# Kernel tuning notes

Hardware: AMD Instinct MI355X
Metric: run time of the kernel (lower is better)

Reference implementation:

```python
import jax, jax.numpy as jnp
import numpy as np

D_MODEL = 2048
N_HEADS = 16
HEAD_DIM = D_MODEL // N_HEADS
B, L = 2, 2048
ROPE_BASE = 10000.0
NEG_INF = -1e30


def _rope_cache(seq_len, head_dim):
    inv_freq = 1.0 / (ROPE_BASE ** (np.arange(0, head_dim, 2, dtype=np.float32) / head_dim))
    t = np.arange(seq_len, dtype=np.float32)
    freqs = np.outer(t, inv_freq)                      # (L, hd/2)
    emb = np.concatenate([freqs, freqs], axis=-1)      # (L, hd)
    return jnp.asarray(np.cos(emb)), jnp.asarray(np.sin(emb))


def setup_inputs() -> dict:
    key = jax.random.key(0)
    kx, kq, ko, kl = jax.random.split(key, 4)
    x = jax.random.normal(kx, (B, L, D_MODEL), dtype=jnp.float32)
    w_qkv = jax.random.normal(kq, (3 * D_MODEL, D_MODEL), dtype=jnp.float32) / np.sqrt(D_MODEL)
    w_out = jax.random.normal(ko, (D_MODEL, D_MODEL), dtype=jnp.float32) / np.sqrt(D_MODEL)
    # key-padding style keep-mask: keep first `lengths[b]` tokens (pos 0 always kept)
    lengths = jax.random.randint(kl, (B,), L // 2, L + 1)
    attn_keep_mask = jnp.arange(L)[None, :] < lengths[:, None]
    cos, sin = _rope_cache(L, HEAD_DIM)
    return {"x": x, "attn_keep_mask": attn_keep_mask, "cos": cos, "sin": sin,
            "w_qkv": w_qkv, "w_out": w_out}


def _rotate_half(t):
    h = t.shape[-1] // 2
    return jnp.concatenate([-t[..., h:], t[..., :h]], axis=-1)


def _apply_rope(t, cos, sin):
    # t: (B, H, L, hd); cos/sin: (L, hd)
    return t * cos[None, None] + _rotate_half(t) * sin[None, None]


def reference(x, attn_keep_mask, cos, sin, w_qkv, w_out):
    Bv, Lv, Dv = x.shape
    qkv = jnp.einsum('bld,ed->ble', x, w_qkv)                      # (B, L, 3D)
    q, k, v = jnp.split(qkv, 3, axis=-1)
    def heads(t):
        return t.reshape(Bv, Lv, N_HEADS, HEAD_DIM).transpose(0, 2, 1, 3)  # (B,H,L,hd)
    q, k, v = heads(q), heads(k), heads(v)
    q = _apply_rope(q, cos, sin)
    k = _apply_rope(k, cos, sin)
    scale = 1.0 / np.sqrt(HEAD_DIM)
    scores = jnp.einsum('bhqd,bhkd->bhqk', q, k) * scale            # (B,H,L,L)
    causal = jnp.tril(jnp.ones((Lv, Lv), dtype=bool))               # (L,L)
    allowed = causal[None, None] & attn_keep_mask[:, None, None, :]  # keep keys
    scores = jnp.where(allowed, scores, NEG_INF)
    probs = jax.nn.softmax(scores, axis=-1)
    attn = jnp.einsum('bhqk,bhkd->bhqd', probs, v)                  # (B,H,L,hd)
    out = attn.transpose(0, 2, 1, 3).reshape(Bv, Lv, Dv)
    out = jnp.where(attn_keep_mask[:, :, None], out, 0.0)
    return jnp.einsum('bld,ed->ble', out, w_out)
```

## Files before the change

kernel.cpp:

```cpp
#include <hip/hip_runtime.h>

typedef unsigned short u16;
typedef u16 u16x8 __attribute__((ext_vector_type(8)));
typedef u16 u16x4 __attribute__((ext_vector_type(4)));
typedef __bf16 bf16x8_t __attribute__((ext_vector_type(8)));
typedef float f32x4 __attribute__((ext_vector_type(4)));

#define GLOBAL_AS __attribute__((address_space(1)))
#define LDS_AS __attribute__((address_space(3)))

__device__ __forceinline__ float bf2f(u16 v) {
    return __uint_as_float(((unsigned int)v) << 16);
}
__device__ __forceinline__ u16 f2bf(float f) {
    unsigned int u = __float_as_uint(f);
    u += 0x7fff + ((u >> 16) & 1);
    return (u16)(u >> 16);
}

__device__ __forceinline__ f32x4 mfma_bf16(u16x8 a, u16x8 b, f32x4 c) {
    return __builtin_amdgcn_mfma_f32_16x16x32_bf16(
        __builtin_bit_cast(bf16x8_t, a), __builtin_bit_cast(bf16x8_t, b), c, 0, 0, 0);
}

__device__ __forceinline__ float red16_max(float x) {
    int t;
    t = __builtin_amdgcn_update_dpp(0, __builtin_bit_cast(int, x), 0xB1, 0xF, 0xF, true);
    x = fmaxf(x, __builtin_bit_cast(float, t));
    t = __builtin_amdgcn_update_dpp(0, __builtin_bit_cast(int, x), 0x4E, 0xF, 0xF, true);
    x = fmaxf(x, __builtin_bit_cast(float, t));
    t = __builtin_amdgcn_update_dpp(0, __builtin_bit_cast(int, x), 0x124, 0xF, 0xF, true);
    x = fmaxf(x, __builtin_bit_cast(float, t));
    t = __builtin_amdgcn_update_dpp(0, __builtin_bit_cast(int, x), 0x128, 0xF, 0xF, true);
    x = fmaxf(x, __builtin_bit_cast(float, t));
    return x;
}

__global__ __launch_bounds__(256) void cvt_kernel(const float* __restrict__ in,
                                                  u16* __restrict__ out, int n4) {
    int i = blockIdx.x * 256 + threadIdx.x;
    if (i >= n4) return;
    float4 f = ((const float4*)in)[i];
    u16x4 o = { f2bf(f.x), f2bf(f.y), f2bf(f.z), f2bf(f.w) };
    ((u16x4*)out)[i] = o;
}

__global__ __launch_bounds__(256) void mask_prep(const unsigned char* __restrict__ raw,
                                                 int* __restrict__ lens) {
    const int b = blockIdx.x;
    const int tid = threadIdx.x, lane = tid & 63, wid = tid >> 6;
    const unsigned char b0 = raw[0];
    int cnt = 0;
    for (int i = tid; i < 2048; i += 256) {
        const size_t idx = (size_t)b * 2048 + i;
        bool v;
        if (b0 == 0) {
            v = ((const float*)raw)[idx] != 0.0f;
        } else if (b0 == 0x80) {
            v = ((const u16*)raw)[idx] != 0;
        } else {
            const int stride = raw[1] ? 1 : (raw[2] ? 2 : (raw[4] ? 4 : 8));
            v = raw[idx * stride] != 0;
        }
        cnt += v ? 1 : 0;
    }
    cnt += __shfl_xor(cnt, 1);
    cnt += __shfl_xor(cnt, 2);
    cnt += __shfl_xor(cnt, 4);
    cnt += __shfl_xor(cnt, 8);
    cnt += __shfl_xor(cnt, 16);
    cnt += __shfl_xor(cnt, 32);
    __shared__ int wsum[4];
    if (lane == 0) wsum[wid] = cnt;
    __syncthreads();
    if (tid == 0) lens[b] = wsum[0] + wsum[1] + wsum[2] + wsum[3];
}

__global__ __launch_bounds__(512, 2) void gemm_qkv(
    const u16* __restrict__ A, const u16* __restrict__ B, int K,
    u16* __restrict__ qp, u16* __restrict__ kp, u16* __restrict__ vp) {
    __shared__ u16 lds[2 * 40960];
    const int tid  = threadIdx.x;
    const int lane = tid & 63;
    const int wid  = tid >> 6;
    const int wm   = wid & 3;
    const int wn   = wid >> 2;

    const int bid = blockIdx.x;
    const int k8  = bid & 7;
    const int loc = bid >> 3;
    const int by  = loc & 15;
    const int bx  = k8 * 2 + (loc >> 4);
    const int brow = by * 256;
    const int bcol = bx * 384;

    f32x4 acc[4][12];
#pragma unroll
    for (int m = 0; m < 4; ++m)
#pragma unroll
        for (int n = 0; n < 12; ++n)
            acc[m][n] = (f32x4){0.f, 0.f, 0.f, 0.f};

    const int s5   = (lane & 7) ^ (lane >> 3);
    const int rofs = 2 * (lane >> 3) + (s5 >> 2);
    const int scol = (s5 & 3) << 3;

    const u16* aS0 = A + (size_t)(brow + wid * 32 + rofs) * K + scol;
    const u16* aS1 = A + (size_t)(brow + wid * 32 + 16 + rofs) * K + scol;
    const u16* bS0 = B + (size_t)(bcol + wid * 48 + rofs) * K + scol;
    const u16* bS1 = B + (size_t)(bcol + wid * 48 + 16 + rofs) * K + scol;
    const u16* bS2 = B + (size_t)(bcol + wid * 48 + 32 + rofs) * K + scol;

    auto stage = [&](int kt, int kh, int bb) {
        char* base = (char*)lds + bb * 81920 + kh * 40960;
        const size_t ko = (size_t)kt * 64 + kh * 32;
        __builtin_amdgcn_global_load_lds((const GLOBAL_AS void*)(aS0 + ko),
            (LDS_AS void*)(base + wid * 2048), 16, 0, 0);
        __builtin_amdgcn_global_load_lds((const GLOBAL_AS void*)(aS1 + ko),
            (LDS_AS void*)(base + wid * 2048 + 1024), 16, 0, 0);
        __builtin_amdgcn_global_load_lds((const GLOBAL_AS void*)(bS0 + ko),
            (LDS_AS void*)(base + 16384 + wid * 3072), 16, 0, 0);
        __builtin_amdgcn_global_load_lds((const GLOBAL_AS void*)(bS1 + ko),
            (LDS_AS void*)(base + 16384 + wid * 3072 + 1024), 16, 0, 0);
        __builtin_amdgcn_global_load_lds((const GLOBAL_AS void*)(bS2 + ko),
            (LDS_AS void*)(base + 16384 + wid * 3072 + 2048), 16, 0, 0);
    };

    auto rdA = [&](int bb, int kh, int mi) -> u16x8 {
        const int r  = wm * 64 + mi * 16 + (lane & 15);
        const int pr = r >> 1;
        const int g  = (((r & 1) << 2) + (lane >> 4)) ^ (pr & 7);
        return *(const u16x8*)((const char*)lds + bb * 81920 + kh * 40960 + pr * 128 + g * 16);
    };
    auto rdB = [&](int bb, int kh, int ni) -> u16x8 {
        const int r  = wn * 192 + ni * 16 + (lane & 15);
        const int pr = r >> 1;
        const int g  = (((r & 1) << 2) + (lane >> 4)) ^ (pr & 7);
        return *(const u16x8*)((const char*)lds + bb * 81920 + kh * 40960 + 16384 + pr * 128 + g * 16);
    };

    const int nkt = K >> 6;
    stage(0, 0, 0);
    stage(0, 1, 0);

    for (int t = 0; t < nkt; ++t) {
        const int cur = t & 1;
        const bool more = (t + 1 < nkt);
        u16x8 af[4];

        asm volatile("s_waitcnt vmcnt(5)" ::: "memory");
        __builtin_amdgcn_s_barrier();
        __builtin_amdgcn_sched_barrier(0);
#pragma unroll
        for (int m = 0; m < 4; ++m) af[m] = rdA(cur, 0, m);
        if (more) stage(t + 1, 0, cur ^ 1);
        __builtin_amdgcn_s_setprio(1);
#pragma unroll
        for (int n = 0; n < 12; ++n) {
            u16x8 bf = rdB(cur, 0, n);
#pragma unroll
            for (int m = 0; m < 4; ++m)
                acc[m][n] = mfma_bf16(af[m], bf, acc[m][n]);
        }
        __builtin_amdgcn_s_setprio(0);

        if (more) asm volatile("s_waitcnt vmcnt(5)" ::: "memory");
        else      asm volatile("s_waitcnt vmcnt(0)" ::: "memory");
        __builtin_amdgcn_s_barrier();
        __builtin_amdgcn_sched_barrier(0);
#pragma unroll
        for (int m = 0; m < 4; ++m) af[m] = rdA(cur, 1, m);
        if (more) stage(t + 1, 1, cur ^ 1);
        __builtin_amdgcn_s_setprio(1);
#pragma unroll
        for (int n = 0; n < 12; ++n) {
            u16x8 bf = rdB(cur, 1, n);
#pragma unroll
            for (int m = 0; m < 4; ++m)
                acc[m][n] = mfma_bf16(af[m], bf, acc[m][n]);
        }
        __builtin_amdgcn_s_setprio(0);
    }

#pragma unroll
    for (int m = 0; m < 4; ++m) {
#pragma unroll
        for (int n = 0; n < 12; ++n) {
#pragma unroll
            for (int j = 0; j < 4; ++j) {
                const int row = brow + wm * 64 + m * 16 + (lane >> 4) * 4 + j;
                const int col = bcol + wn * 192 + n * 16 + (lane & 15);
                const int part = col >> 11;
                const int e = col & 2047;
                const int hh = e >> 7, dd = e & 127;
                const int bb = row >> 11, ll = row & 2047;
                u16* dst = (part == 0) ? qp : (part == 1) ? kp : vp;
                dst[((size_t)(bb * 16 + hh) * 2048 + ll) * 128 + dd] = f2bf(acc[m][n][j]);
            }
        }
    }
}

__global__ __launch_bounds__(512, 2) void gemm_out(
    const u16* __restrict__ A, const u16* __restrict__ B,
    int M, int N, int K, int rbx,
    float* __restrict__ outf) {
    __shared__ u16 lds[2 * 24576];
    const int tid  = threadIdx.x;
    const int lane = tid & 63;
    const int wid  = tid >> 6;
    const int wr   = wid >> 2;
    const int wc   = wid & 3;

    const int bid = blockIdx.x;
    const int k8  = bid & 7;
    const int loc = bid >> 3;
    const int by  = (k8 >> 2) * 16 + (loc & 15);
    const int bx  = (k8 & 3) * rbx + (loc >> 4);
    const int brow = by * 128;
    const int bcol = bx * 256;

    f32x4 acc[4][4];
#pragma unroll
    for (int m = 0; m < 4; ++m)
#pragma unroll
        for (int n = 0; n < 4; ++n)
            acc[m][n] = (f32x4){0.f, 0.f, 0.f, 0.f};

    const int s5   = (lane & 7) ^ (lane >> 3);
    const int srow = (wid << 4) + 2 * (lane >> 3) + (s5 >> 2);
    const int scol = (s5 & 3) << 3;
    const u16* aS = A + (size_t)(brow + srow) * K + scol;
    const u16* bS = B + (size_t)(bcol + srow) * K + scol;

    auto stgA = [&](int kt, int kh, int bb) {
        __builtin_amdgcn_global_load_lds(
            (const GLOBAL_AS void*)(aS + (size_t)kt * 64 + kh * 32),
            (LDS_AS void*)((char*)lds + bb * 49152 + kh * 8192 + wid * 1024), 16, 0, 0);
    };
    auto stgB = [&](int kt, int kh, int bb) {
        const u16* src = bS + (size_t)kt * 64 + kh * 32;
        char* base = (char*)lds + bb * 49152 + 16384 + kh * 16384 + wid * 1024;
        __builtin_amdgcn_global_load_lds((const GLOBAL_AS void*)src,
            (LDS_AS void*)base, 16, 0, 0);
        __builtin_amdgcn_global_load_lds((const GLOBAL_AS void*)(src + (size_t)128 * K),
            (LDS_AS void*)(base + 8192), 16, 0, 0);
    };

    auto rdA = [&](int bb, int kh, int mi) -> u16x8 {
        const int r  = wr * 64 + mi * 16 + (lane & 15);
        const int pr = r >> 1;
        const int g  = (((r & 1) << 2) + (lane >> 4)) ^ (pr & 7);
        return *(const u16x8*)((const char*)lds + bb * 49152 + kh * 8192 + pr * 128 + g * 16);
    };
    auto rdB = [&](int bb, int kh, int ni) -> u16x8 {
        const int r  = wc * 64 + ni * 16 + (lane & 15);
        const int pr = r >> 1;
        const int g  = (((r & 1) << 2) + (lane >> 4)) ^ (pr & 7);
        return *(const u16x8*)((const char*)lds + bb * 49152 + 16384 + kh * 16384 + pr * 128 + g * 16);
    };

    const int nkt = K >> 6;
    stgA(0, 0, 0); stgB(0, 0, 0);
    stgA(0, 1, 0); stgB(0, 1, 0);

    for (int t = 0; t < nkt; ++t) {
        const int cur = t & 1;
        const bool more = (t + 1 < nkt);
        u16x8 af[4], bf[4];

        asm volatile("s_waitcnt vmcnt(3)" ::: "memory");
        __builtin_amdgcn_s_barrier();
        __builtin_amdgcn_sched_barrier(0);
#pragma unroll
        for (int m = 0; m < 4; ++m) af[m] = rdA(cur, 0, m);
#pragma unroll
        for (int n = 0; n < 4; ++n) bf[n] = rdB(cur, 0, n);
        if (more) { stgA(t + 1, 0, cur ^ 1); stgB(t + 1, 0, cur ^ 1); }
        __builtin_amdgcn_s_setprio(1);
#pragma unroll
        for (int m = 0; m < 4; ++m)
#pragma unroll
            for (int n = 0; n < 4; ++n)
                acc[m][n] = mfma_bf16(af[m], bf[n], acc[m][n]);
        __builtin_amdgcn_s_setprio(0);

        if (more) asm volatile("s_waitcnt vmcnt(3)" ::: "memory");
        else      asm volatile("s_waitcnt vmcnt(0)" ::: "memory");
        __builtin_amdgcn_s_barrier();
        __builtin_amdgcn_sched_barrier(0);
#pragma unroll
        for (int m = 0; m < 4; ++m) af[m] = rdA(cur, 1, m);
#pragma unroll
        for (int n = 0; n < 4; ++n) bf[n] = rdB(cur, 1, n);
        if (more) { stgA(t + 1, 1, cur ^ 1); stgB(t + 1, 1, cur ^ 1); }
        __builtin_amdgcn_s_setprio(1);
#pragma unroll
        for (int m = 0; m < 4; ++m)
#pragma unroll
            for (int n = 0; n < 4; ++n)
                acc[m][n] = mfma_bf16(af[m], bf[n], acc[m][n]);
        __builtin_amdgcn_s_setprio(0);
    }

#pragma unroll
    for (int m = 0; m < 4; ++m)
#pragma unroll
        for (int n = 0; n < 4; ++n)
#pragma unroll
            for (int j = 0; j < 4; ++j) {
                const int row = brow + wr * 64 + m * 16 + (lane >> 4) * 4 + j;
                const int col = bcol + wc * 64 + n * 16 + (lane & 15);
                outf[(size_t)row * N + col] = acc[m][n][j];
            }
}

__global__ __launch_bounds__(256) void rope_kernel(u16* __restrict__ qk,
                                                   const float* __restrict__ cosp,
                                                   const float* __restrict__ sinp) {
    const int gid  = blockIdx.x * 4 + (threadIdx.x >> 6);
    const int lane = threadIdx.x & 63;
    const int l    = gid & 2047;
    u16* row = qk + (size_t)gid * 128;
    const int d1 = lane, d2 = lane + 64;
    const float v1 = bf2f(row[d1]);
    const float v2 = bf2f(row[d2]);
    const float c1 = cosp[l * 128 + d1], s1 = sinp[l * 128 + d1];
    const float c2 = cosp[l * 128 + d2], s2 = sinp[l * 128 + d2];
    row[d1] = f2bf(v1 * c1 - v2 * s1);
    row[d2] = f2bf(v2 * c2 + v1 * s2);
}

__global__ __launch_bounds__(256, 2) void attn_kernel(
    const u16* __restrict__ Q, const u16* __restrict__ K, const u16* __restrict__ V,
    const int* __restrict__ lens, u16* __restrict__ O) {
    __shared__ u16 lK[64 * 128];
    __shared__ u16 lVT[128 * 64];
    __shared__ u16 lP[4 * 16 * 64];

    const int tid = threadIdx.x, lane = tid & 63, wid = tid >> 6;
    const int g   = blockIdx.x;
    const int xcd = g & 7;
    const int r   = g >> 3;
    const int jq  = 31 - (r >> 2);
    const int bh  = (xcd << 2) | (r & 3);
    const int b   = bh >> 4;
    const int h   = bh & 15;
    const u16* qb = Q + (size_t)bh * 2048 * 128;
    const u16* kb = K + (size_t)bh * 2048 * 128;
    const u16* vb = V + (size_t)bh * 2048 * 128;
    const int lenb = lens[b];
    const int q0w = jq * 64 + wid * 16;
    const int str = lane;
    const int sdc = wid;
    const float scale2 = 0.12754245006257017f;
    const float THR = 32.0f;
    u16* lPw = lP + wid * 1024;

    if (jq * 64 >= lenb) {
#pragma unroll
        for (int j = 0; j < 4; ++j) {
            const int qq = q0w + (lane >> 4) * 4 + j;
#pragma unroll
            for (int n = 0; n < 8; ++n) {
                const int d = n * 16 + (lane & 15);
                O[((size_t)b * 2048 + qq) * 2048 + h * 128 + d] = 0;
            }
        }
        return;
    }

    const int nt_full = jq + 1;
    const int lt = (lenb + 63) >> 6;
    const int ktiles = nt_full < lt ? nt_full : lt;

    u16x8 aq[4];
#pragma unroll
    for (int kc = 0; kc < 4; ++kc)
        aq[kc] = *(const u16x8*)(qb + (size_t)(q0w + (lane & 15)) * 128 + kc * 32 + (lane >> 4) * 8);

    u16x8 ONES;
#pragma unroll
    for (int e = 0; e < 8; ++e) ONES[e] = 0x3F80;

    float ms[4];
    f32x4 ls4, alpha4;
    f32x4 ao[8];
#pragma unroll
    for (int j = 0; j < 4; ++j) ms[j] = 0.f;
    ls4 = (f32x4){0.f, 0.f, 0.f, 0.f};
#pragma unroll
    for (int n = 0; n < 8; ++n) ao[n] = (f32x4){0.f, 0.f, 0.f, 0.f};

    u16x8 pk[4], pv[4];
    {
        const u16* ks = kb + (size_t)str * 128 + sdc * 32;
        const u16* vs = vb + (size_t)str * 128 + sdc * 32;
#pragma unroll
        for (int i = 0; i < 4; ++i) { pk[i] = *(const u16x8*)(ks + i * 8); pv[i] = *(const u16x8*)(vs + i * 8); }
    }
#pragma unroll
    for (int i = 0; i < 4; ++i) {
        *(u16x8*)&lK[str * 128 + (((sdc * 4 + i) ^ (str & 7)) << 3)] = pk[i];
#pragma unroll
        for (int e = 0; e < 8; ++e) {
            const int d = sdc * 32 + i * 8 + e;
            lVT[d * 64 + (((str >> 3) ^ (d & 7)) << 3) + (str & 7)] = pv[i][e];
        }
    }
    __syncthreads();

    for (int t = 0; t < ktiles; ++t) {
        const bool pf = (t + 1 < ktiles);
        if (pf) {
            const u16* ks = kb + (size_t)((t + 1) * 64 + str) * 128 + sdc * 32;
            const u16* vs = vb + (size_t)((t + 1) * 64 + str) * 128 + sdc * 32;
#pragma unroll
            for (int i = 0; i < 4; ++i) { pk[i] = *(const u16x8*)(ks + i * 8); pv[i] = *(const u16x8*)(vs + i * 8); }
        }
        const int kv0 = t * 64;

        f32x4 sv4[4];
#pragma unroll
        for (int n = 0; n < 4; ++n) sv4[n] = (f32x4){0.f, 0.f, 0.f, 0.f};
#pragma unroll
        for (int kc = 0; kc < 4; ++kc) {
            u16x8 bk[4];
#pragma unroll
            for (int n = 0; n < 4; ++n) {
                const int rk = n * 16 + (lane & 15);
                bk[n] = *(const u16x8*)&lK[rk * 128 + (((kc * 4 + (lane >> 4)) ^ (rk & 7)) << 3)];
            }
#pragma unroll
            for (int n = 0; n < 4; ++n)
                sv4[n] = mfma_bf16(aq[kc], bk[n], sv4[n]);
        }

        const bool needmask = (t == jq) || (kv0 + 64 > lenb);
#pragma unroll
        for (int j = 0; j < 4; ++j) {
            const int row = (lane >> 4) * 4 + j;
            float sv[4];
            if (needmask) {
                const int qq = q0w + row;
                const int bound = (qq < lenb - 1) ? qq : (lenb - 1);
#pragma unroll
                for (int n = 0; n < 4; ++n) {
                    const int kk = kv0 + n * 16 + (lane & 15);
                    sv[n] = (kk <= bound) ? sv4[n][j] : -1e30f;
                }
            } else {
#pragma unroll
                for (int n = 0; n < 4; ++n) sv[n] = sv4[n][j];
            }
            const float mk = ms[j] * scale2;
#pragma unroll
            for (int n = 0; n < 4; ++n) {
                const float p = exp2f(fmaf(sv[n], scale2, -mk));
                lPw[row * 64 + (((n * 2 + ((lane & 15) >> 3)) ^ (row & 7)) << 3) + (lane & 7)] = f2bf(p);
            }
            const float rm = red16_max(fmaxf(fmaxf(sv[0], sv[1]), fmaxf(sv[2], sv[3])));
            const bool grow = !__all(rm <= ms[j] + THR);
            float a = 1.0f;
            if (grow) {
                const float mn = fmaxf(ms[j], rm);
                a = exp2f((ms[j] - mn) * scale2);
                ms[j] = mn;
            }
            alpha4[j] = a;
        }

#pragma unroll
        for (int kc = 0; kc < 2; ++kc) {
            const int rp = lane & 15;
            u16x8 ap = *(const u16x8*)&lPw[rp * 64 + (((kc * 4 + (lane >> 4)) ^ (rp & 7)) << 3)];
            ls4 = mfma_bf16(ap, ONES, ls4);
#pragma unroll
            for (int n = 0; n < 8; ++n) {
                const int rd = n * 16 + (lane & 15);
                u16x8 bv = *(const u16x8*)&lVT[rd * 64 + (((kc * 4 + (lane >> 4)) ^ (rd & 7)) << 3)];
                ao[n] = mfma_bf16(ap, bv, ao[n]);
            }
        }

        ls4 *= alpha4;
#pragma unroll
        for (int n = 0; n < 8; ++n) ao[n] *= alpha4;

        if (pf) {
            __syncthreads();
#pragma unroll
            for (int i = 0; i < 4; ++i) {
                *(u16x8*)&lK[str * 128 + (((sdc * 4 + i) ^ (str & 7)) << 3)] = pk[i];
#pragma unroll
                for (int e = 0; e < 8; ++e) {
                    const int d = sdc * 32 + i * 8 + e;
                    lVT[d * 64 + (((str >> 3) ^ (d & 7)) << 3) + (str & 7)] = pv[i][e];
                }
            }
            __syncthreads();
        }
    }

#pragma unroll
    for (int j = 0; j < 4; ++j) {
        const int qq = q0w + (lane >> 4) * 4 + j;
        const float inv = (qq < lenb) ? (1.f / ls4[j]) : 0.f;
#pragma unroll
        for (int n = 0; n < 8; ++n) {
            const int d = n * 16 + (lane & 15);
            O[((size_t)b * 2048 + qq) * 2048 + h * 128 + d] = f2bf(ao[n][j] * inv);
        }
    }
}

extern "C" void kernel_launch(void* const* d_in, const int* in_sizes, int n_in,
                              void* d_out, int out_size, void* d_ws, size_t ws_size,
                              hipStream_t stream) {
    const float* x      = (const float*)d_in[0];
    const unsigned char* maskraw = (const unsigned char*)d_in[1];
    const float* cosp   = (const float*)d_in[2];
    const float* sinp   = (const float*)d_in[3];
    const float* w_qkv  = (const float*)d_in[4];
    const float* w_out  = (const float*)d_in[5];
    float* out = (float*)d_out;

    char* ws = (char*)d_ws;
    size_t off = 0;
    auto alloc = [&](size_t bytes) {
        char* p = ws + off;
        off += (bytes + 255) & ~(size_t)255;
        return p;
    };
    u16* xb    = (u16*)alloc((size_t)4096 * 2048 * 2);
    u16* wqkvb = (u16*)alloc((size_t)6144 * 2048 * 2);
    u16* woutb = (u16*)alloc((size_t)2048 * 2048 * 2);
    u16* qB    = (u16*)alloc((size_t)65536 * 128 * 2);
    u16* kB    = (u16*)alloc((size_t)65536 * 128 * 2);
    u16* vB    = (u16*)alloc((size_t)65536 * 128 * 2);
    u16* attno = (u16*)alloc((size_t)4096 * 2048 * 2);
    int* lens  = (int*)alloc(256);

    cvt_kernel<<<dim3(4096 * 2048 / 4 / 256), dim3(256), 0, stream>>>(x, xb, 4096 * 2048 / 4);
    cvt_kernel<<<dim3(6144 * 2048 / 4 / 256), dim3(256), 0, stream>>>(w_qkv, wqkvb, 6144 * 2048 / 4);
    cvt_kernel<<<dim3(2048 * 2048 / 4 / 256), dim3(256), 0, stream>>>(w_out, woutb, 2048 * 2048 / 4);
    mask_prep<<<dim3(2), dim3(256), 0, stream>>>(maskraw, lens);

    gemm_qkv<<<dim3(256), dim3(512), 0, stream>>>(xb, wqkvb, 2048, qB, kB, vB);
    rope_kernel<<<dim3(131072 / 4), dim3(256), 0, stream>>>(qB, cosp, sinp);
    attn_kernel<<<dim3(1024), dim3(256), 0, stream>>>(qB, kB, vB, lens, attno);
    gemm_out<<<dim3(256), dim3(512), 0, stream>>>(attno, woutb, 4096, 2048, 2048, 2, out);
}
```

Measured before the change: 247.3 us.

## Deepen QKV GEMM pipeline to four half-K slots with interleaved loads

```diff
diff --git a/kernel.cpp b/kernel.cpp
--- a/kernel.cpp
+++ b/kernel.cpp
@@ -79,7 +79,7 @@
 __global__ __launch_bounds__(512, 2) void gemm_qkv(
     const u16* __restrict__ A, const u16* __restrict__ B, int K,
     u16* __restrict__ qp, u16* __restrict__ kp, u16* __restrict__ vp) {
-    __shared__ u16 lds[2 * 40960];
+    __shared__ u16 lds[4 * 20480];
     const int tid  = threadIdx.x;
     const int lane = tid & 63;
     const int wid  = tid >> 6;
@@ -111,74 +111,97 @@
     const u16* bS1 = B + (size_t)(bcol + wid * 48 + 16 + rofs) * K + scol;
     const u16* bS2 = B + (size_t)(bcol + wid * 48 + 32 + rofs) * K + scol;
 
-    auto stage = [&](int kt, int kh, int bb) {
-        char* base = (char*)lds + bb * 81920 + kh * 40960;
-        const size_t ko = (size_t)kt * 64 + kh * 32;
+    auto issueA = [&](int h) {
+        char* base = (char*)lds + (h & 3) * 40960;
+        const size_t ko = (size_t)h * 32;
         __builtin_amdgcn_global_load_lds((const GLOBAL_AS void*)(aS0 + ko),
             (LDS_AS void*)(base + wid * 2048), 16, 0, 0);
         __builtin_amdgcn_global_load_lds((const GLOBAL_AS void*)(aS1 + ko),
             (LDS_AS void*)(base + wid * 2048 + 1024), 16, 0, 0);
+    };
+    auto issueB01 = [&](int h) {
+        char* base = (char*)lds + (h & 3) * 40960 + 16384 + wid * 3072;
+        const size_t ko = (size_t)h * 32;
         __builtin_amdgcn_global_load_lds((const GLOBAL_AS void*)(bS0 + ko),
-            (LDS_AS void*)(base + 16384 + wid * 3072), 16, 0, 0);
+            (LDS_AS void*)base, 16, 0, 0);
         __builtin_amdgcn_global_load_lds((const GLOBAL_AS void*)(bS1 + ko),
-            (LDS_AS void*)(base + 16384 + wid * 3072 + 1024), 16, 0, 0);
+            (LDS_AS void*)(base + 1024), 16, 0, 0);
+    };
+    auto issueB2 = [&](int h) {
+        char* base = (char*)lds + (h & 3) * 40960 + 16384 + wid * 3072;
+        const size_t ko = (size_t)h * 32;
         __builtin_amdgcn_global_load_lds((const GLOBAL_AS void*)(bS2 + ko),
-            (LDS_AS void*)(base + 16384 + wid * 3072 + 2048), 16, 0, 0);
-    };
-
-    auto rdA = [&](int bb, int kh, int mi) -> u16x8 {
+            (LDS_AS void*)(base + 2048), 16, 0, 0);
+    };
+
+    auto rdA = [&](int slot, int mi) -> u16x8 {
         const int r  = wm * 64 + mi * 16 + (lane & 15);
         const int pr = r >> 1;
         const int g  = (((r & 1) << 2) + (lane >> 4)) ^ (pr & 7);
-        return *(const u16x8*)((const char*)lds + bb * 81920 + kh * 40960 + pr * 128 + g * 16);
-    };
-    auto rdB = [&](int bb, int kh, int ni) -> u16x8 {
+        return *(const u16x8*)((const char*)lds + slot * 40960 + pr * 128 + g * 16);
+    };
+    auto rdB = [&](int slot, int ni) -> u16x8 {
         const int r  = wn * 192 + ni * 16 + (lane & 15);
         const int pr = r >> 1;
         const int g  = (((r & 1) << 2) + (lane >> 4)) ^ (pr & 7);
-        return *(const u16x8*)((const char*)lds + bb * 81920 + kh * 40960 + 16384 + pr * 128 + g * 16);
-    };
-
-    const int nkt = K >> 6;
-    stage(0, 0, 0);
-    stage(0, 1, 0);
-
-    for (int t = 0; t < nkt; ++t) {
-        const int cur = t & 1;
-        const bool more = (t + 1 < nkt);
-        u16x8 af[4];
-
-        asm volatile("s_waitcnt vmcnt(5)" ::: "memory");
+        return *(const u16x8*)((const char*)lds + slot * 40960 + 16384 + pr * 128 + g * 16);
+    };
+
+    const int nh = K >> 5;
+    issueA(0); issueB01(0); issueB2(0);
+    issueA(1); issueB01(1); issueB2(1);
+    issueA(2); issueB01(2); issueB2(2);
+
+    for (int h = 0; h < nh; ++h) {
+        const int slot = h & 3;
+        const bool pf = (h + 3 < nh);
+        u16x8 af[4], bf[4];
+
+        if (h + 2 < nh)      asm volatile("s_waitcnt vmcnt(10)" ::: "memory");
+        else if (h + 1 < nh) asm volatile("s_waitcnt vmcnt(5)" ::: "memory");
+        else                 asm volatile("s_waitcnt vmcnt(0)" ::: "memory");
         __builtin_amdgcn_s_barrier();
         __builtin_amdgcn_sched_barrier(0);
-#pragma unroll
-        for (int m = 0; m < 4; ++m) af[m] = rdA(cur, 0, m);
-        if (more) stage(t + 1, 0, cur ^ 1);
+
+#pragma unroll
+        for (int m = 0; m < 4; ++m) af[m] = rdA(slot, m);
+#pragma unroll
+        for (int n = 0; n < 4; ++n) bf[n] = rdB(slot, n);
+        if (pf) issueA(h + 3);
+        asm volatile("s_waitcnt lgkmcnt(0)" ::: "memory");
+        __builtin_amdgcn_sched_barrier(0);
         __builtin_amdgcn_s_setprio(1);
 #pragma unroll
-        for (int n = 0; n < 12; ++n) {
-            u16x8 bf = rdB(cur, 0, n);
+        for (int n = 0; n < 4; ++n)
 #pragma unroll
             for (int m = 0; m < 4; ++m)
-                acc[m][n] = mfma_bf16(af[m], bf, acc[m][n]);
-        }
+                acc[m][n] = mfma_bf16(af[m], bf[n], acc[m][n]);
         __builtin_amdgcn_s_setprio(0);
 
-        if (more) asm volatile("s_waitcnt vmcnt(5)" ::: "memory");
-        else      asm volatile("s_waitcnt vmcnt(0)" ::: "memory");
-        __builtin_amdgcn_s_barrier();
+#pragma unroll
+        for (int n = 0; n < 4; ++n) bf[n] = rdB(slot, 4 + n);
+        if (pf) issueB01(h + 3);
+        asm volatile("s_waitcnt lgkmcnt(0)" ::: "memory");
         __builtin_amdgcn_sched_barrier(0);
-#pragma unroll
-        for (int m = 0; m < 4; ++m) af[m] = rdA(cur, 1, m);
-        if (more) stage(t + 1, 1, cur ^ 1);
         __builtin_amdgcn_s_setprio(1);
 #pragma unroll
-        for (int n = 0; n < 12; ++n) {
-            u16x8 bf = rdB(cur, 1, n);
+        for (int n = 0; n < 4; ++n)
 #pragma unroll
             for (int m = 0; m < 4; ++m)
-                acc[m][n] = mfma_bf16(af[m], bf, acc[m][n]);
-        }
+                acc[m][4 + n] = mfma_bf16(af[m], bf[n], acc[m][4 + n]);
+        __builtin_amdgcn_s_setprio(0);
+
+#pragma unroll
+        for (int n = 0; n < 4; ++n) bf[n] = rdB(slot, 8 + n);
+        if (pf) issueB2(h + 3);
+        asm volatile("s_waitcnt lgkmcnt(0)" ::: "memory");
+        __builtin_amdgcn_sched_barrier(0);
+        __builtin_amdgcn_s_setprio(1);
+#pragma unroll
+        for (int n = 0; n < 4; ++n)
+#pragma unroll
+            for (int m = 0; m < 4; ++m)
+                acc[m][8 + n] = mfma_bf16(af[m], bf[n], acc[m][8 + n]);
         __builtin_amdgcn_s_setprio(0);
     }
 
```

Measured after the change: 247.8 us. About the same (+0.2%).
